# Kernel tuning notes

Hardware: AMD Instinct MI355X
Metric: run time of the kernel (lower is better)

The kernel has to match this reference:

```python
import math
import jax, jax.numpy as jnp
import numpy as np

NU = 0.01  # kinematic viscosity (init kwarg)
DT = 0.01  # Euler step size (init kwarg)


def _ddx(f):
    # central difference, periodic, last axis
    return (jnp.roll(f, -1, axis=-1) - jnp.roll(f, 1, axis=-1)) * 0.5


def _ddy(f):
    return (jnp.roll(f, -1, axis=-2) - jnp.roll(f, 1, axis=-2)) * 0.5


def _laplacian(f):
    return (jnp.roll(f, 1, axis=-1) + jnp.roll(f, -1, axis=-1)
            + jnp.roll(f, 1, axis=-2) + jnp.roll(f, -1, axis=-2) - 4.0 * f)


def _poisson_fft(rhs):
    # spectral Poisson solve on periodic domain: lap(phi) = rhs
    B, H, W = rhs.shape
    rhs_f = jnp.fft.rfft2(rhs)                                   # [B, H, W//2+1]
    ky = jnp.fft.fftfreq(H, d=1.0 / H).reshape(H, 1)             # integer freqs
    kx = jnp.fft.rfftfreq(W, d=1.0 / W).reshape(1, W // 2 + 1)
    k2 = jnp.maximum(ky ** 2 + kx ** 2, 1e-10)
    k2 = k2.at[0, 0].set(1.0)
    phi_f = rhs_f / (-4.0 * math.pi ** 2 * k2)
    phi_f = phi_f.at[:, 0, 0].set(0.0)
    return jnp.fft.irfft2(phi_f, s=(H, W))


def _l2_normalize(f):
    # matches F.normalize(f.flatten(1), dim=1): L2 over all non-batch dims, eps=1e-12
    norm = jnp.sqrt(jnp.sum(f * f, axis=(-2, -1), keepdims=True))
    return f / jnp.maximum(norm, 1e-12)


def setup_inputs() -> dict:
    key = jax.random.key(0)
    k1, k2, k3, k4 = jax.random.split(key, 4)
    B, H, W = 8, 1024, 1024
    x = jax.random.normal(k1, (B, 3, H, W), dtype=jnp.float32)
    beta_t = jax.random.uniform(k2, (B,), dtype=jnp.float32)
    f_u = jax.random.normal(k3, (B, H, W), dtype=jnp.float32)
    f_v = jax.random.normal(k4, (B, H, W), dtype=jnp.float32)
    return {"x": x, "beta_t": beta_t, "f_u": f_u, "f_v": f_v}


def reference(x, beta_t, f_u, f_v):
    u, v, p = x[:, 0], x[:, 1], x[:, 2]

    adv_u = u * _ddx(u) + v * _ddy(u)
    adv_v = u * _ddx(v) + v * _ddy(v)
    diff_u = NU * _laplacian(u)
    diff_v = NU * _laplacian(v)
    dp_dx, dp_dy = _ddx(p), _ddy(p)

    sqrt_beta = jnp.sqrt(beta_t).reshape(-1, 1, 1)

    # 3-step noise smoothing then global L2 normalization
    for _ in range(3):
        f_u = f_u + 0.1 * _laplacian(f_u)
        f_v = f_v + 0.1 * _laplacian(f_v)
    f_u = _l2_normalize(f_u)
    f_v = _l2_normalize(f_v)

    u_new = u + DT * (-adv_u + diff_u - dp_dx) + sqrt_beta * f_u
    v_new = v + DT * (-adv_v + diff_v - dp_dy) + sqrt_beta * f_v

    # pseudo-spectral projection to enforce incompressibility
    div = _ddx(u_new) + _ddy(v_new)
    p_corr = _poisson_fft(div)
    u_new = u_new - _ddx(p_corr)
    v_new = v_new - _ddy(p_corr)
    p_new = p + p_corr

    return jnp.stack([u_new, v_new, p_new], axis=1)
```

## Files before the change

kernel.cpp:

```cpp
#include <hip/hip_runtime.h>

#define BB 8
#define HH 1024
#define WW 1024
#define HW (HH*WW)
#define PI_F 3.14159265358979323846f

static __device__ __forceinline__ int wrapm(int i, int n) { return (i == 0) ? n - 1 : i - 1; }
static __device__ __forceinline__ int wrapp(int i, int n) { return (i == n - 1) ? 0 : i + 1; }

static __device__ __forceinline__ void gload16(const float* g, float* l)
{
    __builtin_amdgcn_global_load_lds(
        (const __attribute__((address_space(1))) void*)g,
        (__attribute__((address_space(3))) void*)l,
        16, 0, 0);
}

__global__ __launch_bounds__(256) void k_twid(float2* __restrict__ tw,
                                              float* __restrict__ nrm)
{
    int tid = blockIdx.x * 256 + threadIdx.x;
    if (tid < 16) nrm[tid] = 0.0f;
    for (int len = 512; len >= 1; len >>= 1) {
        int off = 1024 - 2 * len;
        float fac = -PI_F / (float)len;
        for (int j = tid; j < len; j += 1024) {
            float sn, cs;
            sincosf(fac * (float)j, &sn, &cs);
            tw[off + j] = make_float2(cs, sn);
        }
    }
}

#define RBAND 8
#define RAWROWS 14

__global__ __launch_bounds__(256) void k_diff3(const float* __restrict__ su,
                                               const float* __restrict__ sv,
                                               float* __restrict__ dst,
                                               float* __restrict__ norms)
{
    __shared__ __align__(16) float A[RAWROWS * WW];
    __shared__ float wsum[4];

    int bid = blockIdx.x;
    int work = (bid & 7) * 256 + (bid >> 3);
    int z = work >> 7;
    int band = work & 127;
    int f = z >> 3, b = z & 7;
    const float* s = ((f == 0) ? su : sv) + (size_t)b * HW;
    float* d = dst + (size_t)z * HW;
    int yb = band * RBAND;
    int tid = threadIdx.x;
    int w = tid >> 6, lane = tid & 63;

    for (int c = w; c < RAWROWS * 4; c += 4) {
        int row = c >> 2, seg = c & 3;
        const float* g = s + (size_t)((yb - 3 + row) & (HH - 1)) * WW
                           + (seg << 8) + (lane << 2);
        gload16(g, &A[(c << 8) + (lane << 2)]);
    }
    __syncthreads();

    const char* Ab = (const char*)A;
    int xq = tid << 4;
    int om = (xq - 16) & 4095;
    int op = (xq + 16) & 4095;

    float r[3][12];
    float i1[3][8];
    float i2[3][6];
    float sq = 0.0f;

    #pragma unroll
    for (int j = 0; j < RAWROWS; ++j) {
        {
            float4 a = *(const float4*)(Ab + j * 4096 + om);
            float4 bq = *(const float4*)(Ab + j * 4096 + xq);
            float4 cq = *(const float4*)(Ab + j * 4096 + op);
            float* rr = r[j % 3];
            rr[0] = a.x; rr[1] = a.y; rr[2] = a.z; rr[3] = a.w;
            rr[4] = bq.x; rr[5] = bq.y; rr[6] = bq.z; rr[7] = bq.w;
            rr[8] = cq.x; rr[9] = cq.y; rr[10] = cq.z; rr[11] = cq.w;
        }
        if (j >= 2) {
            const float* ru = r[(j - 2) % 3];
            const float* rc = r[(j - 1) % 3];
            const float* rd = r[j % 3];
            float* o = i1[(j - 1) % 3];
            #pragma unroll
            for (int k = 0; k < 8; ++k) {
                float c0 = rc[k + 2];
                o[k] = c0 + 0.1f * (rc[k + 1] + rc[k + 3] + ru[k + 2] + rd[k + 2] - 4.0f * c0);
            }
        }
        if (j >= 4) {
            const float* u = i1[(j - 3) % 3];
            const float* c = i1[(j - 2) % 3];
            const float* dd = i1[(j - 1) % 3];
            float* o = i2[(j - 2) % 3];
            #pragma unroll
            for (int k = 0; k < 6; ++k) {
                float c0 = c[k + 1];
                o[k] = c0 + 0.1f * (c[k] + c[k + 2] + u[k + 1] + dd[k + 1] - 4.0f * c0);
            }
        }
        if (j >= 6) {
            const float* u = i2[(j - 4) % 3];
            const float* c = i2[(j - 3) % 3];
            const float* dd = i2[(j - 2) % 3];
            float4 o;
            float* op4 = (float*)&o;
            #pragma unroll
            for (int k = 0; k < 4; ++k) {
                float c0 = c[k + 1];
                op4[k] = c0 + 0.1f * (c[k] + c[k + 2] + u[k + 1] + dd[k + 1] - 4.0f * c0);
            }
            *(float4*)(d + (size_t)(yb + j - 6) * WW + (tid << 2)) = o;
            sq += o.x * o.x + o.y * o.y + o.z * o.z + o.w * o.w;
        }
    }

    #pragma unroll
    for (int o = 32; o > 0; o >>= 1) sq += __shfl_down(sq, o, 64);
    if (lane == 0) wsum[w] = sq;
    __syncthreads();
    if (tid == 0)
        atomicAdd(&norms[z], wsum[0] + wsum[1] + wsum[2] + wsum[3]);
}

__global__ __launch_bounds__(256) void k_star(const float* __restrict__ X,
                                              const float* __restrict__ beta,
                                              const float* __restrict__ F,
                                              const float* __restrict__ norms,
                                              float* __restrict__ UV)
{
    int b = blockIdx.y;
    int y = blockIdx.x;
    int tid = threadIdx.x;
    int lane = tid & 63;
    int xq = tid << 2;
    const float* u = X + (size_t)(b * 3 + 0) * HW;
    const float* v = X + (size_t)(b * 3 + 1) * HW;
    const float* p = X + (size_t)(b * 3 + 2) * HW;
    int yr = y * WW, ym = wrapm(y, HH) * WW, yp = wrapp(y, HH) * WW;

    float4 ucq = *(const float4*)(u + yr + xq);
    float4 uuq = *(const float4*)(u + ym + xq);
    float4 udq = *(const float4*)(u + yp + xq);
    float4 vcq = *(const float4*)(v + yr + xq);
    float4 vuq = *(const float4*)(v + ym + xq);
    float4 vdq = *(const float4*)(v + yp + xq);
    float4 pcq = *(const float4*)(p + yr + xq);
    float4 puq = *(const float4*)(p + ym + xq);
    float4 pdq = *(const float4*)(p + yp + xq);
    float4 fuq = *(const float4*)(F + (size_t)(0 * BB + b) * HW + yr + xq);
    float4 fvq = *(const float4*)(F + (size_t)(1 * BB + b) * HW + yr + xq);

    float ulf = __shfl_up(ucq.w, 1, 64), urt = __shfl_down(ucq.x, 1, 64);
    float vlf = __shfl_up(vcq.w, 1, 64), vrt = __shfl_down(vcq.x, 1, 64);
    float plf = __shfl_up(pcq.w, 1, 64), prt = __shfl_down(pcq.x, 1, 64);
    if (lane == 0)  { int xm = (xq - 1) & (WW - 1); ulf = u[yr + xm]; vlf = v[yr + xm]; plf = p[yr + xm]; }
    if (lane == 63) { int xp = (xq + 4) & (WW - 1); urt = u[yr + xp]; vrt = v[yr + xp]; prt = p[yr + xp]; }

    float ue[6] = { ulf, ucq.x, ucq.y, ucq.z, ucq.w, urt };
    float ve[6] = { vlf, vcq.x, vcq.y, vcq.z, vcq.w, vrt };
    float pe[6] = { plf, pcq.x, pcq.y, pcq.z, pcq.w, prt };
    float uu_[4] = { uuq.x, uuq.y, uuq.z, uuq.w };
    float ud_[4] = { udq.x, udq.y, udq.z, udq.w };
    float vu_[4] = { vuq.x, vuq.y, vuq.z, vuq.w };
    float vd_[4] = { vdq.x, vdq.y, vdq.z, vdq.w };
    float pu_[4] = { puq.x, puq.y, puq.z, puq.w };
    float pd_[4] = { pdq.x, pdq.y, pdq.z, pdq.w };
    float fu_[4] = { fuq.x, fuq.y, fuq.z, fuq.w };
    float fv_[4] = { fvq.x, fvq.y, fvq.z, fvq.w };

    float sb = sqrtf(beta[b]);
    float inu = 1.0f / fmaxf(sqrtf(norms[b]), 1e-12f);
    float inv = 1.0f / fmaxf(sqrtf(norms[BB + b]), 1e-12f);

    float4 un4, vn4;
    float* unp = (float*)&un4;
    float* vnp = (float*)&vn4;
    #pragma unroll
    for (int k = 0; k < 4; ++k) {
        float ucc = ue[k + 1], vcc = ve[k + 1];
        float adv_u = ucc * (0.5f * (ue[k + 2] - ue[k])) + vcc * (0.5f * (ud_[k] - uu_[k]));
        float adv_v = ucc * (0.5f * (ve[k + 2] - ve[k])) + vcc * (0.5f * (vd_[k] - vu_[k]));
        float lap_u = ue[k] + ue[k + 2] + uu_[k] + ud_[k] - 4.0f * ucc;
        float lap_v = ve[k] + ve[k + 2] + vu_[k] + vd_[k] - 4.0f * vcc;
        float dpdx = 0.5f * (pe[k + 2] - pe[k]);
        float dpdy = 0.5f * (pd_[k] - pu_[k]);
        unp[k] = ucc + 0.01f * (-adv_u + 0.01f * lap_u - dpdx) + sb * fu_[k] * inu;
        vnp[k] = vcc + 0.01f * (-adv_v + 0.01f * lap_v - dpdy) + sb * fv_[k] * inv;
    }

    *(float4*)(UV + (size_t)(0 * BB + b) * HW + yr + xq) = un4;
    *(float4*)(UV + (size_t)(1 * BB + b) * HW + yr + xq) = vn4;
}

static __device__ __forceinline__ void fft_dif2(float2* d, const float2* tw)
{
    int t = threadIdx.x;
    for (int s = 9; s >= 0; --s) {
        int len = 1 << s;
        int off = 1024 - 2 * len;
        __syncthreads();
        #pragma unroll
        for (int k = 0; k < 2; ++k) {
            int bt = t + (k << 8);
            int j = bt & (len - 1);
            int i = ((bt >> s) << (s + 1)) | j;
            float2 u = d[i], v = d[i + len], w = tw[off + j];
            d[i] = make_float2(u.x + v.x, u.y + v.y);
            float dr = u.x - v.x, di = u.y - v.y;
            d[i + len] = make_float2(dr * w.x - di * w.y, dr * w.y + di * w.x);
        }
    }
}

static __device__ __forceinline__ void fft_dit_inv2(float2* d, const float2* tw)
{
    int t = threadIdx.x;
    for (int s = 0; s <= 9; ++s) {
        int len = 1 << s;
        int off = 1024 - 2 * len;
        __syncthreads();
        #pragma unroll
        for (int k = 0; k < 2; ++k) {
            int bt = t + (k << 8);
            int j = bt & (len - 1);
            int i = ((bt >> s) << (s + 1)) | j;
            float2 u = d[i], v = d[i + len], w = tw[off + j];
            float tr = v.x * w.x + v.y * w.y;
            float ti = v.y * w.x - v.x * w.y;
            d[i] = make_float2(u.x + tr, u.y + ti);
            d[i + len] = make_float2(u.x - tr, u.y - ti);
        }
    }
}

__global__ __launch_bounds__(256) void k_divfft(const float* __restrict__ UV,
                                                float2* __restrict__ dst,
                                                const float2* __restrict__ tw)
{
    __shared__ __align__(16) float2 data[1024];
    __shared__ __align__(16) float2 twl[1024];
    __shared__ __align__(16) float us0[1024], us1[1024];
    int y = blockIdx.x, q = blockIdx.y;
    int b0 = 2 * q, b1 = 2 * q + 1;
    int tid = threadIdx.x, w = tid >> 6, lane = tid & 63;
    int yr = y * WW, ym = ((y - 1) & (HH - 1)) * WW, yp = ((y + 1) & (HH - 1)) * WW;
    const float* u0 = UV + (size_t)b0 * HW;
    const float* v0 = UV + (size_t)(BB + b0) * HW;
    const float* u1 = UV + (size_t)b1 * HW;
    const float* v1 = UV + (size_t)(BB + b1) * HW;

    gload16(u0 + yr + (w << 8) + (lane << 2), &us0[(w << 8) + (lane << 2)]);
    gload16(u1 + yr + (w << 8) + (lane << 2), &us1[(w << 8) + (lane << 2)]);

    for (int j = tid; j < 1024; j += 256) twl[j] = tw[j];

    int xq = tid << 2;
    float4 v0u = *(const float4*)(v0 + ym + xq);
    float4 v0d = *(const float4*)(v0 + yp + xq);
    float4 v1u = *(const float4*)(v1 + ym + xq);
    float4 v1d = *(const float4*)(v1 + yp + xq);
    __syncthreads();

    float4 c0 = *(const float4*)&us0[xq];
    float4 c1 = *(const float4*)&us1[xq];
    float lf0 = us0[(xq - 1) & 1023], rt0 = us0[(xq + 4) & 1023];
    float lf1 = us1[(xq - 1) & 1023], rt1 = us1[(xq + 4) & 1023];
    float u0e[6] = { lf0, c0.x, c0.y, c0.z, c0.w, rt0 };
    float u1e[6] = { lf1, c1.x, c1.y, c1.z, c1.w, rt1 };
    float v0u_[4] = { v0u.x, v0u.y, v0u.z, v0u.w };
    float v0d_[4] = { v0d.x, v0d.y, v0d.z, v0d.w };
    float v1u_[4] = { v1u.x, v1u.y, v1u.z, v1u.w };
    float v1d_[4] = { v1d.x, v1d.y, v1d.z, v1d.w };
    #pragma unroll
    for (int k = 0; k < 4; ++k) {
        float d0 = 0.5f * (u0e[k + 2] - u0e[k]) + 0.5f * (v0d_[k] - v0u_[k]);
        float d1 = 0.5f * (u1e[k + 2] - u1e[k]) + 0.5f * (v1d_[k] - v1u_[k]);
        data[xq + k] = make_float2(d0, d1);
    }

    fft_dif2(data, twl);
    __syncthreads();
    size_t base = (size_t)((q << 10) + y) << 10;
    float4* dst4 = (float4*)(dst + base);
    float4* dat4 = (float4*)data;
    dst4[2 * tid] = dat4[2 * tid];
    dst4[2 * tid + 1] = dat4[2 * tid + 1];
}

__global__ __launch_bounds__(256) void k_fft_poisson(float2* __restrict__ data_g,
                                                     const float2* __restrict__ tw)
{
    __shared__ __align__(16) float2 data[1024];
    __shared__ __align__(16) float2 twl[1024];
    int r = blockIdx.x;
    int i = r & 1023;
    int kx = __brev((unsigned)i) >> 22;
    int fx = (kx < 512) ? kx : kx - 1024;
    float fx2 = (float)(fx * fx);
    size_t base = (size_t)r * 1024;
    int tid = threadIdx.x, w = tid >> 6, lane = tid & 63;

    const float* g = (const float*)(data_g + base);
    for (int c = w; c < 8; c += 4)
        gload16(g + (c << 8) + (lane << 2), ((float*)data) + (c << 8) + (lane << 2));
    for (int j = tid; j < 1024; j += 256) twl[j] = tw[j];

    fft_dif2(data, twl);
    __syncthreads();
    const float c = -1.0f / (4.0f * PI_F * PI_F * 1024.0f * 1024.0f);
    for (int k = tid; k < 1024; k += 256) {
        int ky = __brev((unsigned)k) >> 22;
        int fy = (ky < 512) ? ky : ky - 1024;
        float k2 = fx2 + (float)(fy * fy);
        float s = (k2 > 0.0f) ? (c / k2) : 0.0f;
        float2 v = data[k];
        data[k] = make_float2(v.x * s, v.y * s);
    }
    fft_dit_inv2(data, twl);
    __syncthreads();
    float4* dg4 = (float4*)(data_g + base);
    float4* dat4 = (float4*)data;
    dg4[2 * tid] = dat4[2 * tid];
    dg4[2 * tid + 1] = dat4[2 * tid + 1];
}

__global__ __launch_bounds__(256) void k_transpose(const float2* __restrict__ src,
                                                   float2* __restrict__ dst)
{
    __shared__ float2 tile[32][33];
    size_t ib = (size_t)blockIdx.z * (size_t)HW;
    int x = blockIdx.x * 32 + threadIdx.x;
    int y0 = blockIdx.y * 32 + threadIdx.y;
    #pragma unroll
    for (int k = 0; k < 4; ++k)
        tile[threadIdx.y + 8 * k][threadIdx.x] = src[ib + (size_t)(y0 + 8 * k) * WW + x];
    __syncthreads();
    int x2 = blockIdx.y * 32 + threadIdx.x;
    int y2 = blockIdx.x * 32 + threadIdx.y;
    #pragma unroll
    for (int k = 0; k < 4; ++k)
        dst[ib + (size_t)(y2 + 8 * k) * WW + x2] = tile[threadIdx.x][threadIdx.y + 8 * k];
}

#define FBAND 4

__global__ __launch_bounds__(256) void k_ifinal(const float2* __restrict__ spec,
                                                const float* __restrict__ UV,
                                                const float* __restrict__ X,
                                                float* __restrict__ out,
                                                const float2* __restrict__ tw)
{
    __shared__ __align__(16) float2 ring[3][1024];
    __shared__ __align__(16) float2 twl[1024];
    int band = blockIdx.x, q = blockIdx.y;
    int b0 = 2 * q, b1 = 2 * q + 1;
    int y0 = band * FBAND;
    int tid = threadIdx.x, w = tid >> 6, lane = tid & 63;

    for (int j = tid; j < 1024; j += 256) twl[j] = tw[j];

    size_t sbase = (size_t)q * HW;
    const float* u0 = UV + (size_t)(0 * BB + b0) * HW;
    const float* v0 = UV + (size_t)(BB + b0) * HW;
    const float* u1 = UV + (size_t)(0 * BB + b1) * HW;
    const float* v1 = UV + (size_t)(BB + b1) * HW;
    const float* p0 = X + (size_t)(b0 * 3 + 2) * HW;
    const float* p1 = X + (size_t)(b1 * 3 + 2) * HW;
    float* o_u0 = out + (size_t)(b0 * 3 + 0) * HW;
    float* o_v0 = out + (size_t)(b0 * 3 + 1) * HW;
    float* o_p0 = out + (size_t)(b0 * 3 + 2) * HW;
    float* o_u1 = out + (size_t)(b1 * 3 + 0) * HW;
    float* o_v1 = out + (size_t)(b1 * 3 + 1) * HW;
    float* o_p1 = out + (size_t)(b1 * 3 + 2) * HW;

    for (int rr = 0; rr < FBAND + 2; ++rr) {
        int yg = (y0 - 1 + rr) & (HH - 1);
        float2* slot = ring[rr % 3];

        __syncthreads();
        const float* g = (const float*)(spec + sbase + (size_t)yg * 1024);
        for (int cch = w; cch < 8; cch += 4)
            gload16(g + (cch << 8) + (lane << 2), ((float*)slot) + (cch << 8) + (lane << 2));

        fft_dit_inv2(slot, twl);
        __syncthreads();

        if (rr >= 2) {
            int ye = y0 + rr - 2;
            const float2* pcn = ring[(rr - 1) % 3];
            const float2* ppm = ring[(rr - 2) % 3];
            const float2* ppp = ring[rr % 3];
            int xq = tid << 2;

            float4 cA = *(const float4*)&pcn[xq];
            float4 cB = *(const float4*)&pcn[xq + 2];
            float4 uA = *(const float4*)&ppm[xq];
            float4 uB = *(const float4*)&ppm[xq + 2];
            float4 dA = *(const float4*)&ppp[xq];
            float4 dB = *(const float4*)&ppp[xq + 2];
            float2 lf = pcn[(xq - 1) & 1023];
            float2 rt = pcn[(xq + 4) & 1023];

            float c0[4] = { cA.x, cA.z, cB.x, cB.z }, c1[4] = { cA.y, cA.w, cB.y, cB.w };
            float um0[4] = { uA.x, uA.z, uB.x, uB.z }, um1[4] = { uA.y, uA.w, uB.y, uB.w };
            float dp0[4] = { dA.x, dA.z, dB.x, dB.z }, dp1[4] = { dA.y, dA.w, dB.y, dB.w };
            float e0[6] = { lf.x, c0[0], c0[1], c0[2], c0[3], rt.x };
            float e1[6] = { lf.y, c1[0], c1[1], c1[2], c1[3], rt.y };

            size_t ro = (size_t)ye * WW + xq;
            float4 u0q = *(const float4*)(u0 + ro);
            float4 v0q = *(const float4*)(v0 + ro);
            float4 u1q = *(const float4*)(u1 + ro);
            float4 v1q = *(const float4*)(v1 + ro);
            float4 p0q = *(const float4*)(p0 + ro);
            float4 p1q = *(const float4*)(p1 + ro);

            float4 ou0, ov0, op0, ou1, ov1, op1;
            #pragma unroll
            for (int k = 0; k < 4; ++k) {
                ((float*)&ou0)[k] = ((float*)&u0q)[k] - 0.5f * (e0[k + 2] - e0[k]);
                ((float*)&ov0)[k] = ((float*)&v0q)[k] - 0.5f * (dp0[k] - um0[k]);
                ((float*)&op0)[k] = ((float*)&p0q)[k] + c0[k];
                ((float*)&ou1)[k] = ((float*)&u1q)[k] - 0.5f * (e1[k + 2] - e1[k]);
                ((float*)&ov1)[k] = ((float*)&v1q)[k] - 0.5f * (dp1[k] - um1[k]);
                ((float*)&op1)[k] = ((float*)&p1q)[k] + c1[k];
            }
            *(float4*)(o_u0 + ro) = ou0;
            *(float4*)(o_v0 + ro) = ov0;
            *(float4*)(o_p0 + ro) = op0;
            *(float4*)(o_u1 + ro) = ou1;
            *(float4*)(o_v1 + ro) = ov1;
            *(float4*)(o_p1 + ro) = op1;
        }
    }
}

extern "C" void kernel_launch(void* const* d_in, const int* in_sizes, int n_in,
                              void* d_out, int out_size, void* d_ws, size_t ws_size,
                              hipStream_t stream)
{
    const float* X    = (const float*)d_in[0];
    const float* beta = (const float*)d_in[1];
    const float* fu   = (const float*)d_in[2];
    const float* fv   = (const float*)d_in[3];
    float* out = (float*)d_out;
    float* ws  = (float*)d_ws;

    float* F1  = ws;
    float* UV  = F1 + (size_t)2 * BB * HW;
    float* Dpf = UV + (size_t)2 * BB * HW;
    float* Cbf = Dpf + (size_t)BB * HW;
    float* TWf = Cbf + (size_t)BB * HW;
    float* NRM = TWf + 2048;
    float2* Dp = (float2*)Dpf;
    float2* Cb = (float2*)Cbf;
    float2* TW = (float2*)TWf;

    k_twid<<<4, 256, 0, stream>>>(TW, NRM);

    dim3 blk(256);
    dim3 tgrid(32, 32, BB / 2), tblk(32, 8);

    k_diff3<<<2048, blk, 0, stream>>>(fu, fv, F1, NRM);
    k_star<<<dim3(HH, BB), blk, 0, stream>>>(X, beta, F1, NRM, UV);

    k_divfft<<<dim3(HH, BB / 2), blk, 0, stream>>>(UV, Cb, TW);
    k_transpose<<<tgrid, tblk, 0, stream>>>(Cb, Dp);
    k_fft_poisson<<<(BB / 2) * HH, blk, 0, stream>>>(Dp, TW);
    k_transpose<<<tgrid, tblk, 0, stream>>>(Dp, Cb);
    k_ifinal<<<dim3(HH / FBAND, BB / 2), blk, 0, stream>>>(Cb, UV, X, out, TW);
}
```

Baseline: 243.7 us.

## Fuse stencil update with divergence and row FFT in banded kernel

Merges the stencil update kernel and the divergence+row-FFT kernel into one kernel. Each block processes a band of 4 rows for a batch pair and recomputes u_new/v_new for the halo rows in registers instead of rereading UV from global memory. Cross-wave edge values are exchanged through small shared arrays. This removes one launch and the UV reread, at the cost of recomputing 2 halo rows per 4-row band, extra syncs, and only 1024 blocks, so each block runs serially through several FFTs.

Measured after the change: 262.7 us. 1.08x slower.

```diff
diff --git a/kernel.cpp b/kernel.cpp
--- a/kernel.cpp
+++ b/kernel.cpp
@@ -5,9 +5,6 @@
 #define WW 1024
 #define HW (HH*WW)
 #define PI_F 3.14159265358979323846f
-
-static __device__ __forceinline__ int wrapm(int i, int n) { return (i == 0) ? n - 1 : i - 1; }
-static __device__ __forceinline__ int wrapp(int i, int n) { return (i == n - 1) ? 0 : i + 1; }
 
 static __device__ __forceinline__ void gload16(const float* g, float* l)
 {
@@ -128,76 +125,6 @@
     __syncthreads();
     if (tid == 0)
         atomicAdd(&norms[z], wsum[0] + wsum[1] + wsum[2] + wsum[3]);
-}
-
-__global__ __launch_bounds__(256) void k_star(const float* __restrict__ X,
-                                              const float* __restrict__ beta,
-                                              const float* __restrict__ F,
-                                              const float* __restrict__ norms,
-                                              float* __restrict__ UV)
-{
-    int b = blockIdx.y;
-    int y = blockIdx.x;
-    int tid = threadIdx.x;
-    int lane = tid & 63;
-    int xq = tid << 2;
-    const float* u = X + (size_t)(b * 3 + 0) * HW;
-    const float* v = X + (size_t)(b * 3 + 1) * HW;
-    const float* p = X + (size_t)(b * 3 + 2) * HW;
-    int yr = y * WW, ym = wrapm(y, HH) * WW, yp = wrapp(y, HH) * WW;
-
-    float4 ucq = *(const float4*)(u + yr + xq);
-    float4 uuq = *(const float4*)(u + ym + xq);
-    float4 udq = *(const float4*)(u + yp + xq);
-    float4 vcq = *(const float4*)(v + yr + xq);
-    float4 vuq = *(const float4*)(v + ym + xq);
-    float4 vdq = *(const float4*)(v + yp + xq);
-    float4 pcq = *(const float4*)(p + yr + xq);
-    float4 puq = *(const float4*)(p + ym + xq);
-    float4 pdq = *(const float4*)(p + yp + xq);
-    float4 fuq = *(const float4*)(F + (size_t)(0 * BB + b) * HW + yr + xq);
-    float4 fvq = *(const float4*)(F + (size_t)(1 * BB + b) * HW + yr + xq);
-
-    float ulf = __shfl_up(ucq.w, 1, 64), urt = __shfl_down(ucq.x, 1, 64);
-    float vlf = __shfl_up(vcq.w, 1, 64), vrt = __shfl_down(vcq.x, 1, 64);
-    float plf = __shfl_up(pcq.w, 1, 64), prt = __shfl_down(pcq.x, 1, 64);
-    if (lane == 0)  { int xm = (xq - 1) & (WW - 1); ulf = u[yr + xm]; vlf = v[yr + xm]; plf = p[yr + xm]; }
-    if (lane == 63) { int xp = (xq + 4) & (WW - 1); urt = u[yr + xp]; vrt = v[yr + xp]; prt = p[yr + xp]; }
-
-    float ue[6] = { ulf, ucq.x, ucq.y, ucq.z, ucq.w, urt };
-    float ve[6] = { vlf, vcq.x, vcq.y, vcq.z, vcq.w, vrt };
-    float pe[6] = { plf, pcq.x, pcq.y, pcq.z, pcq.w, prt };
-    float uu_[4] = { uuq.x, uuq.y, uuq.z, uuq.w };
-    float ud_[4] = { udq.x, udq.y, udq.z, udq.w };
-    float vu_[4] = { vuq.x, vuq.y, vuq.z, vuq.w };
-    float vd_[4] = { vdq.x, vdq.y, vdq.z, vdq.w };
-    float pu_[4] = { puq.x, puq.y, puq.z, puq.w };
-    float pd_[4] = { pdq.x, pdq.y, pdq.z, pdq.w };
-    float fu_[4] = { fuq.x, fuq.y, fuq.z, fuq.w };
-    float fv_[4] = { fvq.x, fvq.y, fvq.z, fvq.w };
-
-    float sb = sqrtf(beta[b]);
-    float inu = 1.0f / fmaxf(sqrtf(norms[b]), 1e-12f);
-    float inv = 1.0f / fmaxf(sqrtf(norms[BB + b]), 1e-12f);
-
-    float4 un4, vn4;
-    float* unp = (float*)&un4;
-    float* vnp = (float*)&vn4;
-    #pragma unroll
-    for (int k = 0; k < 4; ++k) {
-        float ucc = ue[k + 1], vcc = ve[k + 1];
-        float adv_u = ucc * (0.5f * (ue[k + 2] - ue[k])) + vcc * (0.5f * (ud_[k] - uu_[k]));
-        float adv_v = ucc * (0.5f * (ve[k + 2] - ve[k])) + vcc * (0.5f * (vd_[k] - vu_[k]));
-        float lap_u = ue[k] + ue[k + 2] + uu_[k] + ud_[k] - 4.0f * ucc;
-        float lap_v = ve[k] + ve[k + 2] + vu_[k] + vd_[k] - 4.0f * vcc;
-        float dpdx = 0.5f * (pe[k + 2] - pe[k]);
-        float dpdy = 0.5f * (pd_[k] - pu_[k]);
-        unp[k] = ucc + 0.01f * (-adv_u + 0.01f * lap_u - dpdx) + sb * fu_[k] * inu;
-        vnp[k] = vcc + 0.01f * (-adv_v + 0.01f * lap_v - dpdy) + sb * fv_[k] * inv;
-    }
-
-    *(float4*)(UV + (size_t)(0 * BB + b) * HW + yr + xq) = un4;
-    *(float4*)(UV + (size_t)(1 * BB + b) * HW + yr + xq) = vn4;
 }
 
 static __device__ __forceinline__ void fft_dif2(float2* d, const float2* tw)
@@ -241,58 +168,162 @@
     }
 }
 
-__global__ __launch_bounds__(256) void k_divfft(const float* __restrict__ UV,
-                                                float2* __restrict__ dst,
-                                                const float2* __restrict__ tw)
+static __device__ __forceinline__ void star_row(
+    const float* __restrict__ u, const float* __restrict__ v,
+    const float* __restrict__ p, const float* __restrict__ Fu,
+    const float* __restrict__ Fv, int y, int xq, int lane,
+    float sb, float inu, float inv, float* un, float* vn)
+{
+    int yr = (y & (HH - 1)) * WW;
+    int ym = ((y - 1) & (HH - 1)) * WW;
+    int yp = ((y + 1) & (HH - 1)) * WW;
+
+    float4 ucq = *(const float4*)(u + yr + xq);
+    float4 uuq = *(const float4*)(u + ym + xq);
+    float4 udq = *(const float4*)(u + yp + xq);
+    float4 vcq = *(const float4*)(v + yr + xq);
+    float4 vuq = *(const float4*)(v + ym + xq);
+    float4 vdq = *(const float4*)(v + yp + xq);
+    float4 pcq = *(const float4*)(p + yr + xq);
+    float4 puq = *(const float4*)(p + ym + xq);
+    float4 pdq = *(const float4*)(p + yp + xq);
+    float4 fuq = *(const float4*)(Fu + yr + xq);
+    float4 fvq = *(const float4*)(Fv + yr + xq);
+
+    float ulf = __shfl_up(ucq.w, 1, 64), urt = __shfl_down(ucq.x, 1, 64);
+    float vlf = __shfl_up(vcq.w, 1, 64), vrt = __shfl_down(vcq.x, 1, 64);
+    float plf = __shfl_up(pcq.w, 1, 64), prt = __shfl_down(pcq.x, 1, 64);
+    if (lane == 0)  { int xm = (xq - 1) & (WW - 1); ulf = u[yr + xm]; vlf = v[yr + xm]; plf = p[yr + xm]; }
+    if (lane == 63) { int xp = (xq + 4) & (WW - 1); urt = u[yr + xp]; vrt = v[yr + xp]; prt = p[yr + xp]; }
+
+    float ue[6] = { ulf, ucq.x, ucq.y, ucq.z, ucq.w, urt };
+    float ve[6] = { vlf, vcq.x, vcq.y, vcq.z, vcq.w, vrt };
+    float pe[6] = { plf, pcq.x, pcq.y, pcq.z, pcq.w, prt };
+    float uu_[4] = { uuq.x, uuq.y, uuq.z, uuq.w };
+    float ud_[4] = { udq.x, udq.y, udq.z, udq.w };
+    float vu_[4] = { vuq.x, vuq.y, vuq.z, vuq.w };
+    float vd_[4] = { vdq.x, vdq.y, vdq.z, vdq.w };
+    float pu_[4] = { puq.x, puq.y, puq.z, puq.w };
+    float pd_[4] = { pdq.x, pdq.y, pdq.z, pdq.w };
+    float fu_[4] = { fuq.x, fuq.y, fuq.z, fuq.w };
+    float fv_[4] = { fvq.x, fvq.y, fvq.z, fvq.w };
+
+    #pragma unroll
+    for (int k = 0; k < 4; ++k) {
+        float ucc = ue[k + 1], vcc = ve[k + 1];
+        float adv_u = ucc * (0.5f * (ue[k + 2] - ue[k])) + vcc * (0.5f * (ud_[k] - uu_[k]));
+        float adv_v = ucc * (0.5f * (ve[k + 2] - ve[k])) + vcc * (0.5f * (vd_[k] - vu_[k]));
+        float lap_u = ue[k] + ue[k + 2] + uu_[k] + ud_[k] - 4.0f * ucc;
+        float lap_v = ve[k] + ve[k + 2] + vu_[k] + vd_[k] - 4.0f * vcc;
+        float dpdx = 0.5f * (pe[k + 2] - pe[k]);
+        float dpdy = 0.5f * (pd_[k] - pu_[k]);
+        un[k] = ucc + 0.01f * (-adv_u + 0.01f * lap_u - dpdx) + sb * fu_[k] * inu;
+        vn[k] = vcc + 0.01f * (-adv_v + 0.01f * lap_v - dpdy) + sb * fv_[k] * inv;
+    }
+}
+
+#define SB 4
+
+__global__ __launch_bounds__(256) void k_stardiv(const float* __restrict__ X,
+                                                 const float* __restrict__ beta,
+                                                 const float* __restrict__ F,
+                                                 const float* __restrict__ norms,
+                                                 float* __restrict__ UV,
+                                                 float2* __restrict__ spec,
+                                                 const float2* __restrict__ tw)
 {
     __shared__ __align__(16) float2 data[1024];
     __shared__ __align__(16) float2 twl[1024];
-    __shared__ __align__(16) float us0[1024], us1[1024];
-    int y = blockIdx.x, q = blockIdx.y;
+    __shared__ float edgeL[2][2][4], edgeR[2][2][4];
+
+    int bid = blockIdx.x;
+    int work = (bid & 7) * 128 + (bid >> 3);
+    int q = work >> 8;
+    int band = work & 255;
+    int y0 = band * SB;
     int b0 = 2 * q, b1 = 2 * q + 1;
     int tid = threadIdx.x, w = tid >> 6, lane = tid & 63;
-    int yr = y * WW, ym = ((y - 1) & (HH - 1)) * WW, yp = ((y + 1) & (HH - 1)) * WW;
-    const float* u0 = UV + (size_t)b0 * HW;
-    const float* v0 = UV + (size_t)(BB + b0) * HW;
-    const float* u1 = UV + (size_t)b1 * HW;
-    const float* v1 = UV + (size_t)(BB + b1) * HW;
-
-    gload16(u0 + yr + (w << 8) + (lane << 2), &us0[(w << 8) + (lane << 2)]);
-    gload16(u1 + yr + (w << 8) + (lane << 2), &us1[(w << 8) + (lane << 2)]);
+    int xq = tid << 2;
 
     for (int j = tid; j < 1024; j += 256) twl[j] = tw[j];
 
-    int xq = tid << 2;
-    float4 v0u = *(const float4*)(v0 + ym + xq);
-    float4 v0d = *(const float4*)(v0 + yp + xq);
-    float4 v1u = *(const float4*)(v1 + ym + xq);
-    float4 v1d = *(const float4*)(v1 + yp + xq);
-    __syncthreads();
-
-    float4 c0 = *(const float4*)&us0[xq];
-    float4 c1 = *(const float4*)&us1[xq];
-    float lf0 = us0[(xq - 1) & 1023], rt0 = us0[(xq + 4) & 1023];
-    float lf1 = us1[(xq - 1) & 1023], rt1 = us1[(xq + 4) & 1023];
-    float u0e[6] = { lf0, c0.x, c0.y, c0.z, c0.w, rt0 };
-    float u1e[6] = { lf1, c1.x, c1.y, c1.z, c1.w, rt1 };
-    float v0u_[4] = { v0u.x, v0u.y, v0u.z, v0u.w };
-    float v0d_[4] = { v0d.x, v0d.y, v0d.z, v0d.w };
-    float v1u_[4] = { v1u.x, v1u.y, v1u.z, v1u.w };
-    float v1d_[4] = { v1d.x, v1d.y, v1d.z, v1d.w };
-    #pragma unroll
-    for (int k = 0; k < 4; ++k) {
-        float d0 = 0.5f * (u0e[k + 2] - u0e[k]) + 0.5f * (v0d_[k] - v0u_[k]);
-        float d1 = 0.5f * (u1e[k + 2] - u1e[k]) + 0.5f * (v1d_[k] - v1u_[k]);
-        data[xq + k] = make_float2(d0, d1);
-    }
-
-    fft_dif2(data, twl);
-    __syncthreads();
-    size_t base = (size_t)((q << 10) + y) << 10;
-    float4* dst4 = (float4*)(dst + base);
-    float4* dat4 = (float4*)data;
-    dst4[2 * tid] = dat4[2 * tid];
-    dst4[2 * tid + 1] = dat4[2 * tid + 1];
+    const float* u0g = X + (size_t)(b0 * 3 + 0) * HW;
+    const float* v0g = X + (size_t)(b0 * 3 + 1) * HW;
+    const float* p0g = X + (size_t)(b0 * 3 + 2) * HW;
+    const float* u1g = X + (size_t)(b1 * 3 + 0) * HW;
+    const float* v1g = X + (size_t)(b1 * 3 + 1) * HW;
+    const float* p1g = X + (size_t)(b1 * 3 + 2) * HW;
+    const float* Fu0 = F + (size_t)(0 * BB + b0) * HW;
+    const float* Fv0 = F + (size_t)(1 * BB + b0) * HW;
+    const float* Fu1 = F + (size_t)(0 * BB + b1) * HW;
+    const float* Fv1 = F + (size_t)(1 * BB + b1) * HW;
+
+    float sb0 = sqrtf(beta[b0]), sb1 = sqrtf(beta[b1]);
+    float inu0 = 1.0f / fmaxf(sqrtf(norms[b0]), 1e-12f);
+    float inv0 = 1.0f / fmaxf(sqrtf(norms[BB + b0]), 1e-12f);
+    float inu1 = 1.0f / fmaxf(sqrtf(norms[b1]), 1e-12f);
+    float inv1 = 1.0f / fmaxf(sqrtf(norms[BB + b1]), 1e-12f);
+
+    float vnA0[4] = {0}, vnB0[4] = {0}, vnC0[4] = {0};
+    float vnA1[4] = {0}, vnB1[4] = {0}, vnC1[4] = {0};
+    float unP0[4] = {0}, unP1[4] = {0}, unC0[4] = {0}, unC1[4] = {0};
+
+    for (int j = 0; j < SB + 2; ++j) {
+        #pragma unroll
+        for (int k = 0; k < 4; ++k) {
+            vnA0[k] = vnB0[k]; vnB0[k] = vnC0[k];
+            vnA1[k] = vnB1[k]; vnB1[k] = vnC1[k];
+            unP0[k] = unC0[k]; unP1[k] = unC1[k];
+        }
+
+        int y = y0 - 1 + j;
+        star_row(u0g, v0g, p0g, Fu0, Fv0, y, xq, lane, sb0, inu0, inv0, unC0, vnC0);
+        star_row(u1g, v1g, p1g, Fu1, Fv1, y, xq, lane, sb1, inu1, inv1, unC1, vnC1);
+
+        if (j >= 1 && j <= SB) {
+            size_t ro = (size_t)y * WW + xq;
+            *(float4*)(UV + (size_t)(0 * BB + b0) * HW + ro) = *(float4*)unC0;
+            *(float4*)(UV + (size_t)(1 * BB + b0) * HW + ro) = *(float4*)vnC0;
+            *(float4*)(UV + (size_t)(0 * BB + b1) * HW + ro) = *(float4*)unC1;
+            *(float4*)(UV + (size_t)(1 * BB + b1) * HW + ro) = *(float4*)vnC1;
+        }
+
+        if (lane == 63) {
+            edgeL[j & 1][0][(w + 1) & 3] = unC0[3];
+            edgeL[j & 1][1][(w + 1) & 3] = unC1[3];
+        }
+        if (lane == 0) {
+            edgeR[j & 1][0][(w + 3) & 3] = unC0[0];
+            edgeR[j & 1][1][(w + 3) & 3] = unC1[0];
+        }
+        __syncthreads();
+
+        if (j >= 2) {
+            int slot = (j - 1) & 1;
+            float lf0 = __shfl_up(unP0[3], 1, 64), rt0 = __shfl_down(unP0[0], 1, 64);
+            float lf1 = __shfl_up(unP1[3], 1, 64), rt1 = __shfl_down(unP1[0], 1, 64);
+            if (lane == 0)  { lf0 = edgeL[slot][0][w]; lf1 = edgeL[slot][1][w]; }
+            if (lane == 63) { rt0 = edgeR[slot][0][w]; rt1 = edgeR[slot][1][w]; }
+            float e0[6] = { lf0, unP0[0], unP0[1], unP0[2], unP0[3], rt0 };
+            float e1[6] = { lf1, unP1[0], unP1[1], unP1[2], unP1[3], rt1 };
+            #pragma unroll
+            for (int k = 0; k < 4; ++k) {
+                float d0 = 0.5f * (e0[k + 2] - e0[k]) + 0.5f * (vnC0[k] - vnA0[k]);
+                float d1 = 0.5f * (e1[k + 2] - e1[k]) + 0.5f * (vnC1[k] - vnA1[k]);
+                data[xq + k] = make_float2(d0, d1);
+            }
+
+            fft_dif2(data, twl);
+            __syncthreads();
+
+            int r = y0 + j - 2;
+            size_t base = (size_t)((q << 10) + r) << 10;
+            float4* dst4 = (float4*)(spec + base);
+            float4* dat4 = (float4*)data;
+            dst4[2 * tid] = dat4[2 * tid];
+            dst4[2 * tid + 1] = dat4[2 * tid + 1];
+        }
+    }
 }
 
 __global__ __launch_bounds__(256) void k_fft_poisson(float2* __restrict__ data_g,
@@ -470,9 +501,8 @@
     dim3 tgrid(32, 32, BB / 2), tblk(32, 8);
 
     k_diff3<<<2048, blk, 0, stream>>>(fu, fv, F1, NRM);
-    k_star<<<dim3(HH, BB), blk, 0, stream>>>(X, beta, F1, NRM, UV);
-
-    k_divfft<<<dim3(HH, BB / 2), blk, 0, stream>>>(UV, Cb, TW);
+    k_stardiv<<<1024, blk, 0, stream>>>(X, beta, F1, NRM, UV, Cb, TW);
+
     k_transpose<<<tgrid, tblk, 0, stream>>>(Cb, Dp);
     k_fft_poisson<<<(BB / 2) * HH, blk, 0, stream>>>(Dp, TW);
     k_transpose<<<tgrid, tblk, 0, stream>>>(Dp, Cb);
```

## Fuse column FFT Poisson solve with in-LDS transpose, removing transpose kernels

Applied to the files above, without the earlier changes.

Replaces the transpose, row-FFT Poisson, transpose sequence with a single kernel that loads 16-column tiles into shared memory, performs per-wavefront column FFT, spectral scaling, and inverse FFT, then writes back in place. This eliminates two full global-memory transpose passes. It trades them for strided 128-byte column-tile accesses and a large LDS footprint with low occupancy. The row wrap indexing in the star kernel is also simplified to bitmasks.

After: 222.9 us. 1.09x faster.

```diff
diff --git a/kernel.cpp b/kernel.cpp
--- a/kernel.cpp
+++ b/kernel.cpp
@@ -5,9 +5,6 @@
 #define WW 1024
 #define HW (HH*WW)
 #define PI_F 3.14159265358979323846f
-
-static __device__ __forceinline__ int wrapm(int i, int n) { return (i == 0) ? n - 1 : i - 1; }
-static __device__ __forceinline__ int wrapp(int i, int n) { return (i == n - 1) ? 0 : i + 1; }
 
 static __device__ __forceinline__ void gload16(const float* g, float* l)
 {
@@ -144,7 +141,7 @@
     const float* u = X + (size_t)(b * 3 + 0) * HW;
     const float* v = X + (size_t)(b * 3 + 1) * HW;
     const float* p = X + (size_t)(b * 3 + 2) * HW;
-    int yr = y * WW, ym = wrapm(y, HH) * WW, yp = wrapp(y, HH) * WW;
+    int yr = y * WW, ym = ((y - 1) & (HH - 1)) * WW, yp = ((y + 1) & (HH - 1)) * WW;
 
     float4 ucq = *(const float4*)(u + yr + xq);
     float4 uuq = *(const float4*)(u + ym + xq);
@@ -295,59 +292,90 @@
     dst4[2 * tid + 1] = dat4[2 * tid + 1];
 }
 
-__global__ __launch_bounds__(256) void k_fft_poisson(float2* __restrict__ data_g,
-                                                     const float2* __restrict__ tw)
-{
-    __shared__ __align__(16) float2 data[1024];
+#define CT 16
+#define CSTR 1026
+
+__global__ __launch_bounds__(1024) void k_colpass(float2* __restrict__ spec,
+                                                  const float2* __restrict__ tw)
+{
+    __shared__ __align__(16) float2 colbuf[CT * CSTR];
     __shared__ __align__(16) float2 twl[1024];
-    int r = blockIdx.x;
-    int i = r & 1023;
+    int tile = blockIdx.x, q = blockIdx.y;
+    int i0 = tile * CT;
+    int tid = threadIdx.x, lane = tid & 63, w = tid >> 6;
+    size_t qb = (size_t)q * HW;
+
+    twl[tid] = tw[tid];
+
+    float2* g = spec + qb;
+    #pragma unroll 4
+    for (int pass = 0; pass < 16; ++pass) {
+        int n = (pass << 10) + tid;
+        int r = n >> 4, c = n & 15;
+        colbuf[c * CSTR + r] = g[(size_t)r * 1024 + i0 + c];
+    }
+    __syncthreads();
+
+    float2* d = colbuf + w * CSTR;
+    int i = i0 + w;
     int kx = __brev((unsigned)i) >> 22;
     int fx = (kx < 512) ? kx : kx - 1024;
     float fx2 = (float)(fx * fx);
-    size_t base = (size_t)r * 1024;
-    int tid = threadIdx.x, w = tid >> 6, lane = tid & 63;
-
-    const float* g = (const float*)(data_g + base);
-    for (int c = w; c < 8; c += 4)
-        gload16(g + (c << 8) + (lane << 2), ((float*)data) + (c << 8) + (lane << 2));
-    for (int j = tid; j < 1024; j += 256) twl[j] = tw[j];
-
-    fft_dif2(data, twl);
-    __syncthreads();
-    const float c = -1.0f / (4.0f * PI_F * PI_F * 1024.0f * 1024.0f);
-    for (int k = tid; k < 1024; k += 256) {
-        int ky = __brev((unsigned)k) >> 22;
+
+    for (int s = 9; s >= 0; --s) {
+        int len = 1 << s, off = 1024 - 2 * len;
+        asm volatile("s_waitcnt lgkmcnt(0)" ::: "memory");
+        __builtin_amdgcn_sched_barrier(0);
+        #pragma unroll
+        for (int k = 0; k < 8; ++k) {
+            int bt = lane + (k << 6);
+            int j = bt & (len - 1);
+            int ii = ((bt >> s) << (s + 1)) | j;
+            float2 u = d[ii], v = d[ii + len], wv = twl[off + j];
+            d[ii] = make_float2(u.x + v.x, u.y + v.y);
+            float dr = u.x - v.x, di = u.y - v.y;
+            d[ii + len] = make_float2(dr * wv.x - di * wv.y, dr * wv.y + di * wv.x);
+        }
+    }
+    asm volatile("s_waitcnt lgkmcnt(0)" ::: "memory");
+    __builtin_amdgcn_sched_barrier(0);
+    const float cc = -1.0f / (4.0f * PI_F * PI_F * 1024.0f * 1024.0f);
+    #pragma unroll
+    for (int k = 0; k < 16; ++k) {
+        int kk = lane + (k << 6);
+        int ky = __brev((unsigned)kk) >> 22;
         int fy = (ky < 512) ? ky : ky - 1024;
         float k2 = fx2 + (float)(fy * fy);
-        float s = (k2 > 0.0f) ? (c / k2) : 0.0f;
-        float2 v = data[k];
-        data[k] = make_float2(v.x * s, v.y * s);
-    }
-    fft_dit_inv2(data, twl);
+        float s = (k2 > 0.0f) ? (cc / k2) : 0.0f;
+        float2 v = d[kk];
+        d[kk] = make_float2(v.x * s, v.y * s);
+    }
+    for (int s = 0; s <= 9; ++s) {
+        int len = 1 << s, off = 1024 - 2 * len;
+        asm volatile("s_waitcnt lgkmcnt(0)" ::: "memory");
+        __builtin_amdgcn_sched_barrier(0);
+        #pragma unroll
+        for (int k = 0; k < 8; ++k) {
+            int bt = lane + (k << 6);
+            int j = bt & (len - 1);
+            int ii = ((bt >> s) << (s + 1)) | j;
+            float2 u = d[ii], v = d[ii + len], wv = twl[off + j];
+            float tr = v.x * wv.x + v.y * wv.y;
+            float ti = v.y * wv.x - v.x * wv.y;
+            d[ii] = make_float2(u.x + tr, u.y + ti);
+            d[ii + len] = make_float2(u.x - tr, u.y - ti);
+        }
+    }
+    asm volatile("s_waitcnt lgkmcnt(0)" ::: "memory");
+    __builtin_amdgcn_sched_barrier(0);
     __syncthreads();
-    float4* dg4 = (float4*)(data_g + base);
-    float4* dat4 = (float4*)data;
-    dg4[2 * tid] = dat4[2 * tid];
-    dg4[2 * tid + 1] = dat4[2 * tid + 1];
-}
-
-__global__ __launch_bounds__(256) void k_transpose(const float2* __restrict__ src,
-                                                   float2* __restrict__ dst)
-{
-    __shared__ float2 tile[32][33];
-    size_t ib = (size_t)blockIdx.z * (size_t)HW;
-    int x = blockIdx.x * 32 + threadIdx.x;
-    int y0 = blockIdx.y * 32 + threadIdx.y;
-    #pragma unroll
-    for (int k = 0; k < 4; ++k)
-        tile[threadIdx.y + 8 * k][threadIdx.x] = src[ib + (size_t)(y0 + 8 * k) * WW + x];
-    __syncthreads();
-    int x2 = blockIdx.y * 32 + threadIdx.x;
-    int y2 = blockIdx.x * 32 + threadIdx.y;
-    #pragma unroll
-    for (int k = 0; k < 4; ++k)
-        dst[ib + (size_t)(y2 + 8 * k) * WW + x2] = tile[threadIdx.x][threadIdx.y + 8 * k];
+
+    #pragma unroll 4
+    for (int pass = 0; pass < 16; ++pass) {
+        int n = (pass << 10) + tid;
+        int r = n >> 4, c = n & 15;
+        g[(size_t)r * 1024 + i0 + c] = colbuf[c * CSTR + r];
+    }
 }
 
 #define FBAND 4
@@ -460,21 +488,16 @@
     float* Cbf = Dpf + (size_t)BB * HW;
     float* TWf = Cbf + (size_t)BB * HW;
     float* NRM = TWf + 2048;
-    float2* Dp = (float2*)Dpf;
     float2* Cb = (float2*)Cbf;
     float2* TW = (float2*)TWf;
 
     k_twid<<<4, 256, 0, stream>>>(TW, NRM);
 
     dim3 blk(256);
-    dim3 tgrid(32, 32, BB / 2), tblk(32, 8);
 
     k_diff3<<<2048, blk, 0, stream>>>(fu, fv, F1, NRM);
     k_star<<<dim3(HH, BB), blk, 0, stream>>>(X, beta, F1, NRM, UV);
-
     k_divfft<<<dim3(HH, BB / 2), blk, 0, stream>>>(UV, Cb, TW);
-    k_transpose<<<tgrid, tblk, 0, stream>>>(Cb, Dp);
-    k_fft_poisson<<<(BB / 2) * HH, blk, 0, stream>>>(Dp, TW);
-    k_transpose<<<tgrid, tblk, 0, stream>>>(Dp, Cb);
+    k_colpass<<<dim3(64, 4), dim3(1024), 0, stream>>>(Cb, TW);
     k_ifinal<<<dim3(HH / FBAND, BB / 2), blk, 0, stream>>>(Cb, UV, X, out, TW);
 }
```
